# Optimization experiments

Hardware: AMD Instinct MI355X
Metric: run time of the kernel (lower is better)

The kernel has to match this reference:

```python
import jax, jax.numpy as jnp
import numpy as np

B, S, HID = 2, 2048, 2048
H, KVH, HD = 16, 8, 128
EPS = 1e-6
ROPE_THETA = 1e6
NEG = -1e9


def setup_inputs() -> dict:
    key = jax.random.key(0)
    ks = jax.random.split(key, 8)
    hidden_states = jax.random.normal(ks[0], (B, S, HID), dtype=jnp.float32)
    # real rotary embeddings, HF layout: concat(freqs, freqs) along last dim
    inv_freq = 1.0 / (ROPE_THETA ** (jnp.arange(0, HD, 2, dtype=jnp.float32) / HD))
    freqs = jnp.arange(S, dtype=jnp.float32)[:, None] * inv_freq[None, :]  # [S, HD/2]
    emb = jnp.concatenate([freqs, freqs], axis=-1)  # [S, HD]
    cos = jnp.broadcast_to(jnp.cos(emb)[None], (B, S, HD)).astype(jnp.float32)
    sin = jnp.broadcast_to(jnp.sin(emb)[None], (B, S, HD)).astype(jnp.float32)
    # additive causal mask [B, 1, S, S]
    causal = jnp.tril(jnp.ones((S, S), dtype=bool))
    attention_mask = jnp.broadcast_to(
        jnp.where(causal, 0.0, NEG).astype(jnp.float32)[None, None], (B, 1, S, S)
    )
    sc_in = 1.0 / np.sqrt(HID)
    sc_o = 1.0 / np.sqrt(H * HD)
    q_kernel = jax.random.normal(ks[1], (HID, H * HD), dtype=jnp.float32) * sc_in
    k_kernel = jax.random.normal(ks[2], (HID, KVH * HD), dtype=jnp.float32) * sc_in
    v_kernel = jax.random.normal(ks[3], (HID, KVH * HD), dtype=jnp.float32) * sc_in
    o_kernel = jax.random.normal(ks[4], (H * HD, HID), dtype=jnp.float32) * sc_o
    q_norm_w = jnp.ones((HD,), dtype=jnp.float32)
    k_norm_w = jnp.ones((HD,), dtype=jnp.float32)
    return dict(hidden_states=hidden_states, cos=cos, sin=sin,
                attention_mask=attention_mask, q_kernel=q_kernel, k_kernel=k_kernel,
                v_kernel=v_kernel, o_kernel=o_kernel, q_norm_w=q_norm_w, k_norm_w=k_norm_w)


def _rms_norm(x, w):
    dt = x.dtype
    xf = x.astype(jnp.float32)
    var = jnp.mean(jnp.square(xf), axis=-1, keepdims=True)
    return (w * (xf * jax.lax.rsqrt(var + EPS))).astype(dt)


def _rotate_half(x):
    x1, x2 = jnp.split(x, 2, axis=-1)
    return jnp.concatenate([-x2, x1], axis=-1)


def _apply_rope(q, k, cos, sin):
    # q,k: [B,H,S,HD]; cos,sin: [B,S,HD] -> unsqueeze head dim
    cos = cos[:, None, :, :]
    sin = sin[:, None, :, :]
    q = q * cos + _rotate_half(q) * sin
    k = k * cos + _rotate_half(k) * sin
    return q, k


def reference(hidden_states, cos, sin, attention_mask, q_kernel, k_kernel,
              v_kernel, o_kernel, q_norm_w, k_norm_w):
    b, s, _ = hidden_states.shape
    groups = H // KVH
    scaling = HD ** -0.5

    q = (hidden_states @ q_kernel).reshape(b, s, H, HD).transpose(0, 2, 1, 3)
    k = (hidden_states @ k_kernel).reshape(b, s, KVH, HD).transpose(0, 2, 1, 3)
    v = (hidden_states @ v_kernel).reshape(b, s, KVH, HD).transpose(0, 2, 1, 3)

    q = _rms_norm(q, q_norm_w)
    k = _rms_norm(k, k_norm_w)
    q, k = _apply_rope(q, k, cos, sin)

    # GQA repeat_kv: [B,KVH,S,HD] -> [B,H,S,HD]
    k = jnp.repeat(k, groups, axis=1)
    v = jnp.repeat(v, groups, axis=1)

    attn = jnp.einsum('bhqd,bhkd->bhqk', q, k) * scaling  # [B,H,S,S]
    attn = attn + jnp.broadcast_to(attention_mask[:, :, :, :s], (b, H, s, s))
    attn = jax.nn.softmax(attn, axis=-1)
    out = jnp.einsum('bhqk,bhkd->bhqd', attn, v)
    out = out.transpose(0, 2, 1, 3).reshape(b, s, H * HD)
    return out @ o_kernel
```

## Files before the change

### kernel.cpp

```cpp
#include <hip/hip_runtime.h>
#include <hip/hip_bf16.h>
#include <stdint.h>

#define S_ 2048
#define H_ 16
#define KVH_ 8
#define HD_ 128

typedef short bf16x8 __attribute__((ext_vector_type(8)));
typedef float f32x4 __attribute__((ext_vector_type(4)));

__device__ __forceinline__ unsigned short f2bf(float f) {
    union { float f; uint32_t u; } v; v.f = f;
    uint32_t u = v.u;
    return (unsigned short)((u + 0x7FFFu + ((u >> 16) & 1u)) >> 16);
}
__device__ __forceinline__ float bf2f(unsigned short s) {
    union { uint32_t u; float f; } v; v.u = ((uint32_t)s) << 16;
    return v.f;
}
__device__ __forceinline__ void gload16(const void* g, void* l) {
    __builtin_amdgcn_global_load_lds(
        (const __attribute__((address_space(1))) unsigned int*)(uintptr_t)g,
        (__attribute__((address_space(3))) unsigned int*)(unsigned int)(uintptr_t)l,
        16, 0, 0);
}
__device__ __forceinline__ float rowred_max(float x) {
    float t;
    t = __int_as_float(__builtin_amdgcn_update_dpp(0, __float_as_int(x), 0x121, 0xF, 0xF, true)); x = fmaxf(x, t);
    t = __int_as_float(__builtin_amdgcn_update_dpp(0, __float_as_int(x), 0x122, 0xF, 0xF, true)); x = fmaxf(x, t);
    t = __int_as_float(__builtin_amdgcn_update_dpp(0, __float_as_int(x), 0x124, 0xF, 0xF, true)); x = fmaxf(x, t);
    t = __int_as_float(__builtin_amdgcn_update_dpp(0, __float_as_int(x), 0x128, 0xF, 0xF, true)); x = fmaxf(x, t);
    return x;
}
__device__ __forceinline__ float rowred_sum(float x) {
    float t;
    t = __int_as_float(__builtin_amdgcn_update_dpp(0, __float_as_int(x), 0x121, 0xF, 0xF, true)); x += t;
    t = __int_as_float(__builtin_amdgcn_update_dpp(0, __float_as_int(x), 0x122, 0xF, 0xF, true)); x += t;
    t = __int_as_float(__builtin_amdgcn_update_dpp(0, __float_as_int(x), 0x124, 0xF, 0xF, true)); x += t;
    t = __int_as_float(__builtin_amdgcn_update_dpp(0, __float_as_int(x), 0x128, 0xF, 0xF, true)); x += t;
    return x;
}

__global__ __launch_bounds__(256) void k_conv(const float* __restrict__ src,
                                              unsigned short* __restrict__ dst, int n4) {
    int stride = gridDim.x * blockDim.x;
    for (int i = blockIdx.x * blockDim.x + threadIdx.x; i < n4; i += stride) {
        float4 f = ((const float4*)src)[i];
        ushort4 o;
        o.x = f2bf(f.x); o.y = f2bf(f.y); o.z = f2bf(f.z); o.w = f2bf(f.w);
        ((ushort4*)dst)[i] = o;
    }
}

__global__ __launch_bounds__(256) void k_transpose(const float* __restrict__ src, int N,
                                                   unsigned short* __restrict__ dst, int K) {
    __shared__ float tile[32][33];
    int n0 = blockIdx.x * 32, k0 = blockIdx.y * 32;
    int tx = threadIdx.x, ty = threadIdx.y;
    #pragma unroll
    for (int j = 0; j < 32; j += 8)
        tile[ty + j][tx] = src[(size_t)(k0 + ty + j) * N + n0 + tx];
    __syncthreads();
    #pragma unroll
    for (int j = 0; j < 32; j += 8)
        dst[(size_t)(n0 + ty + j) * K + k0 + tx] = f2bf(tile[tx][ty + j]);
}

__global__ __launch_bounds__(256) void k_vtrans(const unsigned short* __restrict__ Cqkv,
                                                unsigned short* __restrict__ Vtg) {
    __shared__ unsigned short tile[32][34];
    const int bkh = blockIdx.z;
    const int b = bkh >> 3, kh = bkh & 7;
    const int s0 = blockIdx.x * 32;
    const int d0 = blockIdx.y * 32;
    const int tx = threadIdx.x, ty = threadIdx.y;
    #pragma unroll
    for (int j = 0; j < 32; j += 8)
        tile[ty + j][tx] = Cqkv[(size_t)(b * S_ + s0 + ty + j) * 4096 + 3072 + kh * HD_ + d0 + tx];
    __syncthreads();
    #pragma unroll
    for (int j = 0; j < 32; j += 8)
        Vtg[((size_t)bkh * HD_ + d0 + ty + j) * S_ + s0 + tx] = tile[tx][ty + j];
}

__global__ __launch_bounds__(512) void k_gemm256(const unsigned short* __restrict__ A,
                                                 const unsigned short* __restrict__ Bt,
                                                 unsigned short* __restrict__ C,
                                                 int M, int N, int K) {
    __shared__ __align__(16) unsigned short As[2][256 * 32];
    __shared__ __align__(16) unsigned short Bs[2][256 * 32];
    const int tid = threadIdx.x;
    const int wave = tid >> 6, lane = tid & 63;
    const int lm = lane & 15, lg = lane >> 4;
    const int wr = wave >> 2, wc = wave & 3;
    const int m0 = blockIdx.y * 256, n0 = blockIdx.x * 256;
    f32x4 acc[8][4] = {};
    const int srow = wave * 16 + (lane >> 2);
    const int sslot = (lane & 3) ^ ((lane >> 3) & 3);
    const unsigned short* gA = A + (size_t)(m0 + srow) * K + sslot * 8;
    const unsigned short* gB = Bt + (size_t)(n0 + srow) * K + sslot * 8;
    const int swz = lg ^ ((lm >> 1) & 3);
    const int NKT = K >> 5;

    auto STAGE = [&](int kt, int buf) {
        const int c = kt * 32;
        char* lA = (char*)&As[buf][0] + wave * 1024;
        char* lB = (char*)&Bs[buf][0] + wave * 1024;
        gload16(gA + c, lA);
        gload16(gA + c + (size_t)128 * K, lA + 8192);
        gload16(gB + c, lB);
        gload16(gB + c + (size_t)128 * K, lB + 8192);
    };
    STAGE(0, 0);
    for (int kt = 0; kt < NKT; ++kt) {
        const int cur = kt & 1;
        if (kt + 1 < NKT) {
            STAGE(kt + 1, cur ^ 1);
            __builtin_amdgcn_sched_barrier(0);
            asm volatile("s_waitcnt vmcnt(4)" ::: "memory");
        } else {
            __builtin_amdgcn_sched_barrier(0);
            asm volatile("s_waitcnt vmcnt(0)" ::: "memory");
        }
        __builtin_amdgcn_s_barrier();
        __builtin_amdgcn_sched_barrier(0);
        bf16x8 bfr[4];
        #pragma unroll
        for (int n = 0; n < 4; n++)
            bfr[n] = *(const bf16x8*)&Bs[cur][(wc * 64 + n * 16 + lm) * 32 + swz * 8];
        __builtin_amdgcn_s_setprio(1);
        #pragma unroll
        for (int m = 0; m < 8; m++) {
            bf16x8 a = *(const bf16x8*)&As[cur][(wr * 128 + m * 16 + lm) * 32 + swz * 8];
            #pragma unroll
            for (int n = 0; n < 4; n++)
                acc[m][n] = __builtin_amdgcn_mfma_f32_16x16x32_bf16(a, bfr[n], acc[m][n], 0, 0, 0);
        }
        __builtin_amdgcn_s_setprio(0);
        __builtin_amdgcn_sched_barrier(0);
        __builtin_amdgcn_s_barrier();
        __builtin_amdgcn_sched_barrier(0);
    }
    #pragma unroll
    for (int m = 0; m < 8; m++) {
        const int row = m0 + wr * 128 + m * 16 + lg * 4;
        #pragma unroll
        for (int n = 0; n < 4; n++) {
            const int col = n0 + wc * 64 + n * 16 + lm;
            #pragma unroll
            for (int i = 0; i < 4; i++)
                C[(size_t)(row + i) * N + col] = f2bf(acc[m][n][i]);
        }
    }
}

template <int OUT_BF16>
__global__ __launch_bounds__(256) void k_gemm(const unsigned short* __restrict__ A,
                                              const unsigned short* __restrict__ Bt,
                                              void* __restrict__ Cv,
                                              int M, int N, int K) {
    __shared__ __align__(16) unsigned short As[128 * 32];
    __shared__ __align__(16) unsigned short Bs[128 * 32];
    const int tid = threadIdx.x;
    const int wave = tid >> 6, lane = tid & 63;
    const int lm = lane & 15, lg = lane >> 4;
    const int m0 = blockIdx.y * 128, n0 = blockIdx.x * 128;
    const int wr = wave >> 1, wc = wave & 1;
    f32x4 acc[4][4] = {};
    const unsigned short* gA = A + (size_t)(m0 + (tid >> 2)) * K + (tid & 3) * 8;
    const unsigned short* gB = Bt + (size_t)(n0 + (tid >> 2)) * K + (tid & 3) * 8;
    char* lA = (char*)As + wave * 1024;
    char* lB = (char*)Bs + wave * 1024;
    for (int k0 = 0; k0 < K; k0 += 32) {
        __syncthreads();
        gload16(gA + k0, lA);
        gload16(gA + k0 + (size_t)64 * K, lA + 4096);
        gload16(gB + k0, lB);
        gload16(gB + k0 + (size_t)64 * K, lB + 4096);
        __syncthreads();
        bf16x8 af[4], bfr[4];
        #pragma unroll
        for (int mi = 0; mi < 4; mi++)
            af[mi] = *(const bf16x8*)&As[(wr * 64 + mi * 16 + lm) * 32 + lg * 8];
        #pragma unroll
        for (int ni = 0; ni < 4; ni++)
            bfr[ni] = *(const bf16x8*)&Bs[(wc * 64 + ni * 16 + lm) * 32 + lg * 8];
        #pragma unroll
        for (int mi = 0; mi < 4; mi++)
            #pragma unroll
            for (int ni = 0; ni < 4; ni++)
                acc[mi][ni] = __builtin_amdgcn_mfma_f32_16x16x32_bf16(af[mi], bfr[ni], acc[mi][ni], 0, 0, 0);
    }
    #pragma unroll
    for (int mi = 0; mi < 4; mi++) {
        #pragma unroll
        for (int ni = 0; ni < 4; ni++) {
            const int row = m0 + wr * 64 + mi * 16 + lg * 4;
            const int col = n0 + wc * 64 + ni * 16 + lm;
            #pragma unroll
            for (int i = 0; i < 4; i++) {
                float v = acc[mi][ni][i];
                if (OUT_BF16) ((unsigned short*)Cv)[(size_t)(row + i) * N + col] = f2bf(v);
                else          ((float*)Cv)[(size_t)(row + i) * N + col] = v;
            }
        }
    }
}

__global__ __launch_bounds__(256) void k_normrope(
    const unsigned short* __restrict__ Cqkv,
    const float* __restrict__ cosb, const float* __restrict__ sinb,
    const float* __restrict__ qw, const float* __restrict__ kw,
    unsigned short* __restrict__ Qb, unsigned short* __restrict__ Kb) {
    const int row = blockIdx.x;
    const int b = row >> 11, s = row & (S_ - 1);
    const int wave = threadIdx.x >> 6, lane = threadIdx.x & 63;
    const float c0 = cosb[(size_t)row * HD_ + lane];
    const float c1 = cosb[(size_t)row * HD_ + lane + 64];
    const float s0 = sinb[(size_t)row * HD_ + lane];
    const float s1 = sinb[(size_t)row * HD_ + lane + 64];
    for (int u = wave; u < 24; u += 4) {
        const int isq = (u < 16);
        const int head = isq ? u : u - 16;
        const unsigned short* x = Cqkv + (size_t)row * 4096 + (isq ? 0 : 2048) + head * HD_;
        float x0 = bf2f(x[lane]), x1 = bf2f(x[lane + 64]);
        float ss = x0 * x0 + x1 * x1;
        #pragma unroll
        for (int o = 32; o >= 1; o >>= 1) ss += __shfl_xor(ss, o, 64);
        float r = rsqrtf(ss * (1.0f / HD_) + 1e-6f);
        const float* wv = isq ? qw : kw;
        float y0 = x0 * r * wv[lane], y1 = x1 * r * wv[lane + 64];
        float o0 = y0 * c0 - y1 * s0;
        float o1 = y1 * c1 + y0 * s1;
        unsigned short* dst = isq ? Qb + ((size_t)(b * H_ + head) * S_ + s) * HD_
                                  : Kb + ((size_t)(b * KVH_ + head) * S_ + s) * HD_;
        dst[lane] = f2bf(o0);
        dst[lane + 64] = f2bf(o1);
    }
}

__global__ __launch_bounds__(256) void k_attn(
    const unsigned short* __restrict__ Qb,
    const unsigned short* __restrict__ Kb,
    const unsigned short* __restrict__ Vtg,
    unsigned short* __restrict__ AO) {
    __shared__ __align__(16) unsigned short Kt[2][64 * 128];
    __shared__ __align__(16) unsigned short Vt[2][128 * 64];
    __shared__ __align__(16) unsigned short Pl[4][16][72];
    const int h = blockIdx.y, b = blockIdx.z;
    const int qi = (b == 0) ? (gridDim.x - 1 - blockIdx.x) : blockIdx.x;
    const int kh = h >> 1;
    const int tid = threadIdx.x, wave = tid >> 6, lane = tid & 63;
    const int lm = lane & 15, lg = lane >> 4;
    const int q0 = qi * 128;
    bf16x8 qf[2][4];
    #pragma unroll
    for (int rg = 0; rg < 2; rg++) {
        const unsigned short* Qp = Qb + ((size_t)(b * H_ + h) * S_ + q0 + wave * 32 + rg * 16 + lm) * HD_;
        #pragma unroll
        for (int d0 = 0; d0 < 4; d0++) qf[rg][d0] = *(const bf16x8*)(Qp + d0 * 32 + lg * 8);
    }
    f32x4 accO[2][8] = {};
    float mrow[2][4], lrow[2][4];
    #pragma unroll
    for (int rg = 0; rg < 2; rg++)
        #pragma unroll
        for (int i = 0; i < 4; i++) { mrow[rg][i] = -1e30f; lrow[rg][i] = 0.f; }
    const unsigned short* Kg = Kb + (size_t)(b * KVH_ + kh) * S_ * HD_;
    const unsigned short* Vg = Vtg + (size_t)(b * KVH_ + kh) * HD_ * S_;
    const int kr = wave * 4 + (lane >> 4);
    const int kc = ((lane & 15) ^ (kr & 7)) * 8;
    const int vr = wave * 8 + (lane >> 3);
    const int vc = ((lane & 7) ^ (vr & 7)) * 8;
    const float scaling = 0.08838834764831845f;
    const int NT = 2 * qi + 2;

    auto STAGE = [&](int t, int buf) {
        const int k0 = t * 64;
        char* lK = (char*)&Kt[buf][0] + wave * 1024;
        char* lV = (char*)&Vt[buf][0] + wave * 1024;
        #pragma unroll
        for (int j = 0; j < 4; ++j) {
            gload16(Kg + (size_t)(k0 + kr + j * 16) * HD_ + kc, lK + j * 4096);
            gload16(Vg + (size_t)(vr + j * 32) * S_ + k0 + vc, lV + j * 4096);
        }
    };
    STAGE(0, 0);
    for (int t = 0; t < NT; ++t) {
        const int cur = t & 1;
        const int k0 = t * 64;
        if (t + 1 < NT) {
            STAGE(t + 1, cur ^ 1);
            __builtin_amdgcn_sched_barrier(0);
            asm volatile("s_waitcnt vmcnt(8)" ::: "memory");
        } else {
            __builtin_amdgcn_sched_barrier(0);
            asm volatile("s_waitcnt vmcnt(0)" ::: "memory");
        }
        __builtin_amdgcn_s_barrier();
        __builtin_amdgcn_sched_barrier(0);
        f32x4 sc[2][4] = {};
        __builtin_amdgcn_s_setprio(1);
        #pragma unroll
        for (int nk = 0; nk < 4; nk++)
            #pragma unroll
            for (int d0 = 0; d0 < 4; d0++) {
                bf16x8 kf = *(const bf16x8*)&Kt[cur][(nk * 16 + lm) * 128 +
                                                    ((d0 * 32 + lg * 8) ^ ((lm & 7) << 3))];
                sc[0][nk] = __builtin_amdgcn_mfma_f32_16x16x32_bf16(qf[0][d0], kf, sc[0][nk], 0, 0, 0);
                sc[1][nk] = __builtin_amdgcn_mfma_f32_16x16x32_bf16(qf[1][d0], kf, sc[1][nk], 0, 0, 0);
            }
        __builtin_amdgcn_s_setprio(0);
        const bool diag = (t >= 2 * qi);
        #pragma unroll
        for (int rg = 0; rg < 2; rg++) {
            const int qrow0 = q0 + wave * 32 + rg * 16;
            float rm[4] = { -1e30f, -1e30f, -1e30f, -1e30f };
            #pragma unroll
            for (int nk = 0; nk < 4; nk++)
                #pragma unroll
                for (int i = 0; i < 4; i++) {
                    float v = sc[rg][nk][i] * scaling;
                    if (diag && (k0 + nk * 16 + lm) > (qrow0 + lg * 4 + i)) v = -1e30f;
                    sc[rg][nk][i] = v;
                    rm[i] = fmaxf(rm[i], v);
                }
            #pragma unroll
            for (int i = 0; i < 4; i++) rm[i] = rowred_max(rm[i]);
            float ps[4], rs[4];
            #pragma unroll
            for (int i = 0; i < 4; i++) {
                float mn = fmaxf(mrow[rg][i], rm[i]);
                ps[i] = __expf(mrow[rg][i] - mn);
                mrow[rg][i] = mn;
                rs[i] = 0.f;
            }
            #pragma unroll
            for (int nk = 0; nk < 4; nk++)
                #pragma unroll
                for (int i = 0; i < 4; i++) {
                    float p = __expf(sc[rg][nk][i] - mrow[rg][i]);
                    rs[i] += p;
                    Pl[wave][lg * 4 + i][nk * 16 + lm] = f2bf(p);
                }
            #pragma unroll
            for (int i = 0; i < 4; i++) rs[i] = rowred_sum(rs[i]);
            #pragma unroll
            for (int i = 0; i < 4; i++) lrow[rg][i] = lrow[rg][i] * ps[i] + rs[i];
            #pragma unroll
            for (int df = 0; df < 8; df++)
                #pragma unroll
                for (int i = 0; i < 4; i++) accO[rg][df][i] *= ps[i];
            __builtin_amdgcn_s_setprio(1);
            #pragma unroll
            for (int kk = 0; kk < 2; kk++) {
                bf16x8 pa = *(const bf16x8*)&Pl[wave][lm][kk * 32 + lg * 8];
                #pragma unroll
                for (int df = 0; df < 8; df++) {
                    bf16x8 vf = *(const bf16x8*)&Vt[cur][(df * 16 + lm) * 64 +
                                                         ((kk * 32 + lg * 8) ^ ((lm & 7) << 3))];
                    accO[rg][df] = __builtin_amdgcn_mfma_f32_16x16x32_bf16(pa, vf, accO[rg][df], 0, 0, 0);
                }
            }
            __builtin_amdgcn_s_setprio(0);
        }
        __builtin_amdgcn_sched_barrier(0);
        __builtin_amdgcn_s_barrier();
        __builtin_amdgcn_sched_barrier(0);
    }
    #pragma unroll
    for (int rg = 0; rg < 2; rg++) {
        unsigned short* Op = AO + ((size_t)b * S_ + q0 + wave * 32 + rg * 16) * (H_ * HD_) + h * HD_;
        #pragma unroll
        for (int df = 0; df < 8; df++)
            #pragma unroll
            for (int i = 0; i < 4; i++) {
                float v = accO[rg][df][i] / lrow[rg][i];
                Op[(size_t)(lg * 4 + i) * (H_ * HD_) + df * 16 + lm] = f2bf(v);
            }
    }
}

extern "C" void kernel_launch(void* const* d_in, const int* in_sizes, int n_in,
                              void* d_out, int out_size, void* d_ws, size_t ws_size,
                              hipStream_t stream) {
    const float* hidden = (const float*)d_in[0];
    const float* cosb = (const float*)d_in[1];
    const float* sinb = (const float*)d_in[2];
    const float* qk = (const float*)d_in[4];
    const float* kk = (const float*)d_in[5];
    const float* vk = (const float*)d_in[6];
    const float* ok = (const float*)d_in[7];
    const float* qw = (const float*)d_in[8];
    const float* kw = (const float*)d_in[9];
    char* ws = (char*)d_ws;
    unsigned short* Xb    = (unsigned short*)ws;
    unsigned short* Wqkvt = (unsigned short*)(ws + (16u << 20));
    unsigned short* Wot   = (unsigned short*)(ws + (32u << 20));
    unsigned short* Cqkv  = (unsigned short*)(ws + (40u << 20));
    unsigned short* Qb  = Xb;
    unsigned short* Kb  = Wqkvt;
    unsigned short* Vtg = (unsigned short*)(ws + (24u << 20));
    unsigned short* AO  = Cqkv;

    k_conv<<<2048, 256, 0, stream>>>(hidden, Xb, (2 * S_ * 2048) / 4);
    k_transpose<<<dim3(64, 64), dim3(32, 8), 0, stream>>>(qk, 2048, Wqkvt, 2048);
    k_transpose<<<dim3(32, 64), dim3(32, 8), 0, stream>>>(kk, 1024, Wqkvt + (size_t)2048 * 2048, 2048);
    k_transpose<<<dim3(32, 64), dim3(32, 8), 0, stream>>>(vk, 1024, Wqkvt + (size_t)3072 * 2048, 2048);
    k_transpose<<<dim3(64, 64), dim3(32, 8), 0, stream>>>(ok, 2048, Wot, 2048);
    k_gemm256<<<dim3(16, 16), 512, 0, stream>>>(Xb, Wqkvt, Cqkv, 4096, 4096, 2048);
    k_vtrans<<<dim3(64, 4, 16), dim3(32, 8), 0, stream>>>(Cqkv, Vtg);
    k_normrope<<<4096, 256, 0, stream>>>(Cqkv, cosb, sinb, qw, kw, Qb, Kb);
    k_attn<<<dim3(16, H_, 2), 256, 0, stream>>>(Qb, Kb, Vtg, AO);
    k_gemm<0><<<dim3(16, 32), 256, 0, stream>>>(AO, Wot, d_out, 4096, 2048, 2048);
}
```

Measured before the change: 269.8 us.

## Reuse pipelined 256-wide GEMM for output projection and add lazy softmax rescaling

The 256-wide double-buffered GEMM kernel is templated on M-tile size and output type. The output projection now uses a 128x256 tile variant with software pipelining, replacing the simpler single-buffered 128x128 GEMM. In attention, the online-softmax rescale of the accumulator and row sum is skipped unless some row max grows by more than 8 across the wave. This removes per-tile exp and multiply work, at the cost of larger unnormalized intermediates, which a threshold of 8 keeps bounded.

```diff
diff --git a/kernel.cpp b/kernel.cpp
--- a/kernel.cpp
+++ b/kernel.cpp
@@ -84,18 +84,20 @@
         Vtg[((size_t)bkh * HD_ + d0 + ty + j) * S_ + s0 + tx] = tile[tx][ty + j];
 }
 
+template <int BM, int OUT_F32>
 __global__ __launch_bounds__(512) void k_gemm256(const unsigned short* __restrict__ A,
                                                  const unsigned short* __restrict__ Bt,
-                                                 unsigned short* __restrict__ C,
+                                                 void* __restrict__ Cv,
                                                  int M, int N, int K) {
-    __shared__ __align__(16) unsigned short As[2][256 * 32];
+    __shared__ __align__(16) unsigned short As[2][BM * 32];
     __shared__ __align__(16) unsigned short Bs[2][256 * 32];
     const int tid = threadIdx.x;
     const int wave = tid >> 6, lane = tid & 63;
     const int lm = lane & 15, lg = lane >> 4;
     const int wr = wave >> 2, wc = wave & 3;
-    const int m0 = blockIdx.y * 256, n0 = blockIdx.x * 256;
-    f32x4 acc[8][4] = {};
+    const int m0 = blockIdx.y * BM, n0 = blockIdx.x * 256;
+    constexpr int MF = BM / 32;
+    f32x4 acc[MF][4] = {};
     const int srow = wave * 16 + (lane >> 2);
     const int sslot = (lane & 3) ^ ((lane >> 3) & 3);
     const unsigned short* gA = A + (size_t)(m0 + srow) * K + sslot * 8;
@@ -108,7 +110,7 @@
         char* lA = (char*)&As[buf][0] + wave * 1024;
         char* lB = (char*)&Bs[buf][0] + wave * 1024;
         gload16(gA + c, lA);
-        gload16(gA + c + (size_t)128 * K, lA + 8192);
+        if constexpr (BM == 256) gload16(gA + c + (size_t)128 * K, lA + 8192);
         gload16(gB + c, lB);
         gload16(gB + c + (size_t)128 * K, lB + 8192);
     };
@@ -118,7 +120,8 @@
         if (kt + 1 < NKT) {
             STAGE(kt + 1, cur ^ 1);
             __builtin_amdgcn_sched_barrier(0);
-            asm volatile("s_waitcnt vmcnt(4)" ::: "memory");
+            if constexpr (BM == 256) asm volatile("s_waitcnt vmcnt(4)" ::: "memory");
+            else                     asm volatile("s_waitcnt vmcnt(3)" ::: "memory");
         } else {
             __builtin_amdgcn_sched_barrier(0);
             asm volatile("s_waitcnt vmcnt(0)" ::: "memory");
@@ -131,8 +134,8 @@
             bfr[n] = *(const bf16x8*)&Bs[cur][(wc * 64 + n * 16 + lm) * 32 + swz * 8];
         __builtin_amdgcn_s_setprio(1);
         #pragma unroll
-        for (int m = 0; m < 8; m++) {
-            bf16x8 a = *(const bf16x8*)&As[cur][(wr * 128 + m * 16 + lm) * 32 + swz * 8];
+        for (int m = 0; m < MF; m++) {
+            bf16x8 a = *(const bf16x8*)&As[cur][(wr * (BM / 2) + m * 16 + lm) * 32 + swz * 8];
             #pragma unroll
             for (int n = 0; n < 4; n++)
                 acc[m][n] = __builtin_amdgcn_mfma_f32_16x16x32_bf16(a, bfr[n], acc[m][n], 0, 0, 0);
@@ -143,66 +146,15 @@
         __builtin_amdgcn_sched_barrier(0);
     }
     #pragma unroll
-    for (int m = 0; m < 8; m++) {
-        const int row = m0 + wr * 128 + m * 16 + lg * 4;
+    for (int m = 0; m < MF; m++) {
+        const int row = m0 + wr * (BM / 2) + m * 16 + lg * 4;
         #pragma unroll
         for (int n = 0; n < 4; n++) {
             const int col = n0 + wc * 64 + n * 16 + lm;
             #pragma unroll
-            for (int i = 0; i < 4; i++)
-                C[(size_t)(row + i) * N + col] = f2bf(acc[m][n][i]);
-        }
-    }
-}
-
-template <int OUT_BF16>
-__global__ __launch_bounds__(256) void k_gemm(const unsigned short* __restrict__ A,
-                                              const unsigned short* __restrict__ Bt,
-                                              void* __restrict__ Cv,
-                                              int M, int N, int K) {
-    __shared__ __align__(16) unsigned short As[128 * 32];
-    __shared__ __align__(16) unsigned short Bs[128 * 32];
-    const int tid = threadIdx.x;
-    const int wave = tid >> 6, lane = tid & 63;
-    const int lm = lane & 15, lg = lane >> 4;
-    const int m0 = blockIdx.y * 128, n0 = blockIdx.x * 128;
-    const int wr = wave >> 1, wc = wave & 1;
-    f32x4 acc[4][4] = {};
-    const unsigned short* gA = A + (size_t)(m0 + (tid >> 2)) * K + (tid & 3) * 8;
-    const unsigned short* gB = Bt + (size_t)(n0 + (tid >> 2)) * K + (tid & 3) * 8;
-    char* lA = (char*)As + wave * 1024;
-    char* lB = (char*)Bs + wave * 1024;
-    for (int k0 = 0; k0 < K; k0 += 32) {
-        __syncthreads();
-        gload16(gA + k0, lA);
-        gload16(gA + k0 + (size_t)64 * K, lA + 4096);
-        gload16(gB + k0, lB);
-        gload16(gB + k0 + (size_t)64 * K, lB + 4096);
-        __syncthreads();
-        bf16x8 af[4], bfr[4];
-        #pragma unroll
-        for (int mi = 0; mi < 4; mi++)
-            af[mi] = *(const bf16x8*)&As[(wr * 64 + mi * 16 + lm) * 32 + lg * 8];
-        #pragma unroll
-        for (int ni = 0; ni < 4; ni++)
-            bfr[ni] = *(const bf16x8*)&Bs[(wc * 64 + ni * 16 + lm) * 32 + lg * 8];
-        #pragma unroll
-        for (int mi = 0; mi < 4; mi++)
-            #pragma unroll
-            for (int ni = 0; ni < 4; ni++)
-                acc[mi][ni] = __builtin_amdgcn_mfma_f32_16x16x32_bf16(af[mi], bfr[ni], acc[mi][ni], 0, 0, 0);
-    }
-    #pragma unroll
-    for (int mi = 0; mi < 4; mi++) {
-        #pragma unroll
-        for (int ni = 0; ni < 4; ni++) {
-            const int row = m0 + wr * 64 + mi * 16 + lg * 4;
-            const int col = n0 + wc * 64 + ni * 16 + lm;
-            #pragma unroll
             for (int i = 0; i < 4; i++) {
-                float v = acc[mi][ni][i];
-                if (OUT_BF16) ((unsigned short*)Cv)[(size_t)(row + i) * N + col] = f2bf(v);
-                else          ((float*)Cv)[(size_t)(row + i) * N + col] = v;
+                if (OUT_F32) ((float*)Cv)[(size_t)(row + i) * N + col] = acc[m][n][i];
+                else ((unsigned short*)Cv)[(size_t)(row + i) * N + col] = f2bf(acc[m][n][i]);
             }
         }
     }
@@ -328,14 +280,20 @@
                 }
             #pragma unroll
             for (int i = 0; i < 4; i++) rm[i] = rowred_max(rm[i]);
-            float ps[4], rs[4];
-            #pragma unroll
-            for (int i = 0; i < 4; i++) {
-                float mn = fmaxf(mrow[rg][i], rm[i]);
-                ps[i] = __expf(mrow[rg][i] - mn);
-                mrow[rg][i] = mn;
-                rs[i] = 0.f;
-            }
+            float g = fmaxf(fmaxf(rm[0] - mrow[rg][0], rm[1] - mrow[rg][1]),
+                            fmaxf(rm[2] - mrow[rg][2], rm[3] - mrow[rg][3]));
+            if (!__all(g <= 8.0f)) {
+                #pragma unroll
+                for (int i = 0; i < 4; i++) {
+                    float mn = fmaxf(mrow[rg][i], rm[i]);
+                    float ps = __expf(mrow[rg][i] - mn);
+                    mrow[rg][i] = mn;
+                    lrow[rg][i] *= ps;
+                    #pragma unroll
+                    for (int df = 0; df < 8; df++) accO[rg][df][i] *= ps;
+                }
+            }
+            float rs[4] = { 0.f, 0.f, 0.f, 0.f };
             #pragma unroll
             for (int nk = 0; nk < 4; nk++)
                 #pragma unroll
@@ -347,11 +305,7 @@
             #pragma unroll
             for (int i = 0; i < 4; i++) rs[i] = rowred_sum(rs[i]);
             #pragma unroll
-            for (int i = 0; i < 4; i++) lrow[rg][i] = lrow[rg][i] * ps[i] + rs[i];
-            #pragma unroll
-            for (int df = 0; df < 8; df++)
-                #pragma unroll
-                for (int i = 0; i < 4; i++) accO[rg][df][i] *= ps[i];
+            for (int i = 0; i < 4; i++) lrow[rg][i] += rs[i];
             __builtin_amdgcn_s_setprio(1);
             #pragma unroll
             for (int kk = 0; kk < 2; kk++) {
@@ -409,9 +363,9 @@
     k_transpose<<<dim3(32, 64), dim3(32, 8), 0, stream>>>(kk, 1024, Wqkvt + (size_t)2048 * 2048, 2048);
     k_transpose<<<dim3(32, 64), dim3(32, 8), 0, stream>>>(vk, 1024, Wqkvt + (size_t)3072 * 2048, 2048);
     k_transpose<<<dim3(64, 64), dim3(32, 8), 0, stream>>>(ok, 2048, Wot, 2048);
-    k_gemm256<<<dim3(16, 16), 512, 0, stream>>>(Xb, Wqkvt, Cqkv, 4096, 4096, 2048);
+    k_gemm256<256, 0><<<dim3(16, 16), 512, 0, stream>>>(Xb, Wqkvt, Cqkv, 4096, 4096, 2048);
     k_vtrans<<<dim3(64, 4, 16), dim3(32, 8), 0, stream>>>(Cqkv, Vtg);
     k_normrope<<<4096, 256, 0, stream>>>(Cqkv, cosb, sinb, qw, kw, Qb, Kb);
     k_attn<<<dim3(16, H_, 2), 256, 0, stream>>>(Qb, Kb, Vtg, AO);
-    k_gemm<0><<<dim3(16, 32), 256, 0, stream>>>(AO, Wot, d_out, 4096, 2048, 2048);
-}
+    k_gemm256<128, 1><<<dim3(8, 32), 512, 0, stream>>>(AO, Wot, d_out, 4096, 2048, 2048);
+}
```

Result: slower. 314.3 us (+16.5%).
